# Kernel tuning notes

Hardware: AMD Instinct MI355X
Metric: run time of the kernel (lower is better)

## Reference

```python
import jax, jax.numpy as jnp
import numpy as np

N, E = 50000, 800000
DIN_N, DIN_E = 64, 64
DO_N, DO_E, H = 32, 32, 4
NEG_SLOPE = 0.01


def setup_inputs() -> dict:
    key = jax.random.key(0)
    ks = jax.random.split(key, 12)
    s = 0.05
    return {
        "nfeats": jax.random.normal(ks[0], (N, DIN_N), jnp.float32),
        "efeats": jax.random.normal(ks[1], (E, DIN_E), jnp.float32),
        "src": jax.random.randint(ks[2], (E,), 0, N, jnp.int32),
        "dst": jax.random.randint(ks[3], (E,), 0, N, jnp.int32),
        "Wn": jax.random.normal(ks[4], (DIN_N, DO_N * H), jnp.float32) * s,
        "bn": jnp.zeros((DO_N * H,), jnp.float32),
        "We": jax.random.normal(ks[5], (DIN_E + 2 * DIN_N, DO_E * H), jnp.float32) * s,
        "Wa": jax.random.normal(ks[6], (DO_E, H), jnp.float32) * s,
        "Won": jax.random.normal(ks[7], (DO_N * H, DO_N), jnp.float32) * s,
        "bon": jnp.zeros((DO_N,), jnp.float32),
        "Woe": jax.random.normal(ks[8], (DO_E * H, DO_E), jnp.float32) * s,
        "boe": jnp.zeros((DO_E,), jnp.float32),
    }


def _egat(nfeats, efeats, src, dst, Wn, bn, We, Wa, Won, bon, Woe, boe):
    # edge attention: concat [h_src, f, h_dst] -> linear(no bias) -> leaky_relu
    stack = jnp.concatenate([nfeats[src], efeats, nfeats[dst]], axis=-1)  # [E, 2Dn+De]
    f = jax.nn.leaky_relu(stack @ We, NEG_SLOPE).reshape(E, H, DO_E)      # [E, H, Fo]
    # fc_attn: [E,H,Fo] @ [Fo,H] -> [E,H,H], summed over last axis -> [E,H]
    a = jnp.einsum("ehf,fk->eh", f, Wa * 1.0) * 0 + (f @ Wa).sum(-1)
    a = (f @ Wa).sum(-1)  # [E, H]
    # projected node features for messages
    nproj = (nfeats @ Wn + bn).reshape(N, H, DO_N)  # [N, H, Do]
    # segment softmax of a over destination nodes
    m = jax.ops.segment_max(a, dst, num_segments=N)  # [N, H]
    m = jnp.where(jnp.isfinite(m), m, 0.0)
    ex = jnp.exp(a - m[dst])                         # [E, H]
    den = jax.ops.segment_sum(ex, dst, num_segments=N)  # [N, H]
    alpha = ex / den[dst]                            # safe: dst has >=1 edge here
    # weighted scatter-sum of src messages
    msg = alpha[:, :, None] * nproj[src]             # [E, H, Do]
    agg = jax.ops.segment_sum(msg, dst, num_segments=N)  # [N, H, Do]
    # zero in-degree nodes keep projected features (DGL update_all semantics)
    deg = jax.ops.segment_sum(jnp.ones((E,), nfeats.dtype), dst, num_segments=N)
    h = jnp.where(deg[:, None, None] > 0, agg, nproj)
    h_out = h.reshape(N, H * DO_N) @ Won + bon
    e_out = f.reshape(E, H * DO_E) @ Woe + boe
    return h_out, e_out


def reference(nfeats, efeats, src, dst, Wn, bn, We, Wa, Won, bon, Woe, boe):
    return _egat(nfeats, efeats, src, dst, Wn, bn, We, Wa, Won, bon, Woe, boe)
```

## Files before the change

kernel.cpp:

```cpp
#include <hip/hip_runtime.h>
#include <hip/hip_bf16.h>


#define NN 50000
#define NE 800000
#define NB ((NN + 255) / 256)

typedef __attribute__((ext_vector_type(8))) __bf16 bf16x8;
typedef __attribute__((ext_vector_type(4))) float f32x4;

__device__ __forceinline__ float lrelu(float x) { return x > 0.f ? x : 0.01f * x; }

__global__ __launch_bounds__(256) void k_count(const int* __restrict__ dst,
                                               int* __restrict__ deg)
{
    int i = blockIdx.x * blockDim.x + threadIdx.x;
    int stride = gridDim.x * blockDim.x;
    for (; i < NE; i += stride) atomicAdd(&deg[dst[i]], 1);
}

__global__ __launch_bounds__(256) void k_scan_blk(const int* __restrict__ deg,
                                                  int* __restrict__ rowptr,
                                                  int* __restrict__ bsum)
{
    __shared__ int wsum[4];
    const int tid = threadIdx.x, lane = tid & 63, wid = tid >> 6;
    const int i = blockIdx.x * 256 + tid;
    int v = (i < NN) ? deg[i] : 0;
    int x = v;
    #pragma unroll
    for (int off = 1; off < 64; off <<= 1) {
        int t = __shfl_up(x, off);
        if (lane >= off) x += t;
    }
    if (lane == 63) wsum[wid] = x;
    __syncthreads();
    if (tid == 0) {
        int s = 0;
        #pragma unroll
        for (int w = 0; w < 4; ++w) { int t = wsum[w]; wsum[w] = s; s += t; }
        bsum[blockIdx.x] = s;
    }
    __syncthreads();
    if (i < NN) rowptr[i] = wsum[wid] + x - v;
}

__global__ __launch_bounds__(256) void k_scan_top(int* __restrict__ bsum,
                                                  int* __restrict__ rowptr)
{
    __shared__ int wsum[4];
    const int tid = threadIdx.x, lane = tid & 63, wid = tid >> 6;
    int v = (tid < NB) ? bsum[tid] : 0;
    int x = v;
    #pragma unroll
    for (int off = 1; off < 64; off <<= 1) {
        int t = __shfl_up(x, off);
        if (lane >= off) x += t;
    }
    if (lane == 63) wsum[wid] = x;
    __syncthreads();
    if (tid == 0) {
        int s = 0;
        #pragma unroll
        for (int w = 0; w < 4; ++w) { int t = wsum[w]; wsum[w] = s; s += t; }
    }
    __syncthreads();
    int excl = wsum[wid] + x - v;
    if (tid < NB) bsum[tid] = excl;
    if (tid == NB - 1) rowptr[NN] = excl + v;
}

__global__ __launch_bounds__(256) void k_scan_add(int* __restrict__ rowptr,
                                                  const int* __restrict__ bsum,
                                                  int* __restrict__ cursor)
{
    const int i = blockIdx.x * 256 + threadIdx.x;
    if (i < NN) {
        int r = rowptr[i] + bsum[blockIdx.x];
        rowptr[i] = r;
        cursor[i] = r;
    }
}

__global__ __launch_bounds__(256) void k_prepw(const float* __restrict__ We,
                                               const float* __restrict__ Wa,
                                               unsigned short* __restrict__ Wefrag,
                                               float* __restrict__ wa_sum)
{
    const int tid = threadIdx.x;
    if (tid < 32) {
        float4 w = *reinterpret_cast<const float4*>(&Wa[tid * 4]);
        wa_sum[tid] = w.x + w.y + w.z + w.w;
    }
    #pragma unroll
    for (int i = 0; i < 32; ++i) {
        int idx = tid * 32 + i;
        int j = idx & 7, l = (idx >> 3) & 63, th = idx >> 9;
        int h = th & 1, t = th >> 1;
        int k = 32 * h + (l >> 4) * 8 + j;
        int c = 16 * t + (l & 15);
        __bf16 b = (__bf16)We[(64 + k) * 128 + c];
        Wefrag[idx] = *reinterpret_cast<unsigned short*>(&b);
    }
}

__global__ __launch_bounds__(256) void k_proj(
    const float* __restrict__ nf, const float* __restrict__ Wn,
    const float* __restrict__ bn, const float* __restrict__ We,
    float* __restrict__ nproj, float* __restrict__ Psrc, float* __restrict__ Pdst)
{
    __shared__ __align__(16) float sA[64 * 68];
    __shared__ __align__(16) float sW[64 * 128];
    const int tid = threadIdx.x;
    const int mode = blockIdx.y;
    const int nBase = blockIdx.x * 64;

    const float* W = (mode == 0) ? Wn : (mode == 1 ? We : We + 128 * 128);
    float* outp = (mode == 0) ? nproj : (mode == 1 ? Psrc : Pdst);

    #pragma unroll
    for (int q = 0; q < 4; ++q) {
        int idx = q * 256 + tid;
        int e = idx >> 4, c4 = idx & 15;
        int row = nBase + e;
        float4 v = make_float4(0.f, 0.f, 0.f, 0.f);
        if (row < NN) v = *reinterpret_cast<const float4*>(&nf[row * 64 + c4 * 4]);
        *reinterpret_cast<float4*>(&sA[e * 68 + c4 * 4]) = v;
    }
    #pragma unroll
    for (int q = 0; q < 8; ++q) {
        int idx = q * 256 + tid;
        *reinterpret_cast<float4*>(&sW[idx * 4]) =
            *reinterpret_cast<const float4*>(&W[idx * 4]);
    }
    __syncthreads();

    const int jt = tid & 15, et = tid >> 4;
    float acc[4][8];
    #pragma unroll
    for (int i = 0; i < 4; ++i)
        #pragma unroll
        for (int j = 0; j < 8; ++j) acc[i][j] = 0.f;

    #pragma unroll 2
    for (int kk4 = 0; kk4 < 16; ++kk4) {
        float4 a4[4];
        #pragma unroll
        for (int i = 0; i < 4; ++i)
            a4[i] = *reinterpret_cast<const float4*>(&sA[(4 * et + i) * 68 + 4 * kk4]);
        #pragma unroll
        for (int c = 0; c < 4; ++c) {
            int kk = 4 * kk4 + c;
            float4 b0 = *reinterpret_cast<const float4*>(&sW[kk * 128 + 4 * jt]);
            float4 b1 = *reinterpret_cast<const float4*>(&sW[kk * 128 + 64 + 4 * jt]);
            #pragma unroll
            for (int i = 0; i < 4; ++i) {
                float av = (&a4[i].x)[c];
                acc[i][0] = fmaf(av, b0.x, acc[i][0]);
                acc[i][1] = fmaf(av, b0.y, acc[i][1]);
                acc[i][2] = fmaf(av, b0.z, acc[i][2]);
                acc[i][3] = fmaf(av, b0.w, acc[i][3]);
                acc[i][4] = fmaf(av, b1.x, acc[i][4]);
                acc[i][5] = fmaf(av, b1.y, acc[i][5]);
                acc[i][6] = fmaf(av, b1.z, acc[i][6]);
                acc[i][7] = fmaf(av, b1.w, acc[i][7]);
            }
        }
    }

    float4 bias0 = make_float4(0.f, 0.f, 0.f, 0.f), bias1 = bias0;
    if (mode == 0) {
        bias0 = *reinterpret_cast<const float4*>(&bn[4 * jt]);
        bias1 = *reinterpret_cast<const float4*>(&bn[64 + 4 * jt]);
    }
    #pragma unroll
    for (int i = 0; i < 4; ++i) {
        int row = nBase + 4 * et + i;
        if (row >= NN) continue;
        float4 r0 = make_float4(acc[i][0] + bias0.x, acc[i][1] + bias0.y,
                                acc[i][2] + bias0.z, acc[i][3] + bias0.w);
        float4 r1 = make_float4(acc[i][4] + bias1.x, acc[i][5] + bias1.y,
                                acc[i][6] + bias1.z, acc[i][7] + bias1.w);
        *reinterpret_cast<float4*>(&outp[row * 128 + 4 * jt]) = r0;
        *reinterpret_cast<float4*>(&outp[row * 128 + 64 + 4 * jt]) = r1;
    }
}

__global__ __launch_bounds__(256) void k_edge(
    const float* __restrict__ ef, const int* __restrict__ src,
    const int* __restrict__ dst,
    const unsigned short* __restrict__ Wefrag, const float* __restrict__ wa_sum,
    const float* __restrict__ Woe, const float* __restrict__ boe,
    const float* __restrict__ Psrc, const float* __restrict__ Pdst,
    int* __restrict__ cursor, int* __restrict__ srcs,
    float* __restrict__ exs, float* __restrict__ e_out)
{
    __shared__ __align__(16) float sf[64 * 132];
    __shared__ __align__(16) float sWoe[128 * 32];
    __shared__ __align__(16) float sboe[32];

    const int tid = threadIdx.x;
    const int w = tid >> 6, l = tid & 63;
    const int g = l >> 4, c16 = l & 15;
    const int eBase = blockIdx.x * 64;
    const int rowBase = eBase + 16 * w;

    #pragma unroll
    for (int q = 0; q < 4; ++q) {
        int idx = q * 256 + tid;
        *reinterpret_cast<float4*>(&sWoe[idx * 4]) =
            *reinterpret_cast<const float4*>(&Woe[idx * 4]);
    }
    if (tid < 32) sboe[tid] = boe[tid];

    int sreg[4], dreg[4];
    #pragma unroll
    for (int r = 0; r < 4; ++r) {
        sreg[r] = src[rowBase + 4 * g + r];
        dreg[r] = dst[rowBase + 4 * g + r];
    }

    bf16x8 afrag[2];
    #pragma unroll
    for (int h = 0; h < 2; ++h) {
        const float* ap = &ef[(size_t)(rowBase + c16) * 64 + 32 * h + 8 * g];
        float4 a0 = *reinterpret_cast<const float4*>(ap);
        float4 a1 = *reinterpret_cast<const float4*>(ap + 4);
        bf16x8 v;
        v[0] = (__bf16)a0.x; v[1] = (__bf16)a0.y;
        v[2] = (__bf16)a0.z; v[3] = (__bf16)a0.w;
        v[4] = (__bf16)a1.x; v[5] = (__bf16)a1.y;
        v[6] = (__bf16)a1.z; v[7] = (__bf16)a1.w;
        afrag[h] = v;
    }

    f32x4 acc[8];
    #pragma unroll
    for (int t = 0; t < 8; ++t) {
        f32x4 z = {0.f, 0.f, 0.f, 0.f};
        acc[t] = z;
        #pragma unroll
        for (int h = 0; h < 2; ++h) {
            bf16x8 b = *reinterpret_cast<const bf16x8*>(
                &Wefrag[((size_t)(t * 2 + h) * 64 + l) * 8]);
            acc[t] = __builtin_amdgcn_mfma_f32_16x16x32_bf16(afrag[h], b, acc[t], 0, 0, 0);
        }
    }

    float a_acc[4][4];
    #pragma unroll
    for (int r = 0; r < 4; ++r)
        #pragma unroll
        for (int h = 0; h < 4; ++h) a_acc[r][h] = 0.f;

    #pragma unroll
    for (int t = 0; t < 8; ++t) {
        int j = 16 * t + c16;
        float waj = wa_sum[j & 31];
        #pragma unroll
        for (int r = 0; r < 4; ++r) {
            float ps = Psrc[(size_t)sreg[r] * 128 + j];
            float pd = Pdst[(size_t)dreg[r] * 128 + j];
            float f = lrelu(acc[t][r] + ps + pd);
            sf[(16 * w + 4 * g + r) * 132 + j] = f;
            a_acc[r][t >> 1] = fmaf(f, waj, a_acc[r][t >> 1]);
        }
    }

    #pragma unroll
    for (int r = 0; r < 4; ++r)
        #pragma unroll
        for (int h = 0; h < 4; ++h) {
            float v = a_acc[r][h];
            v += __shfl_xor(v, 1);
            v += __shfl_xor(v, 2);
            v += __shfl_xor(v, 4);
            v += __shfl_xor(v, 8);
            a_acc[r][h] = v;
        }

    #pragma unroll
    for (int r = 0; r < 4; ++r) {
        int pos = 0;
        if (c16 == 0) pos = atomicAdd(&cursor[dreg[r]], 1);
        pos = __shfl(pos, g * 16);
        if (c16 == 0) srcs[pos] = sreg[r];
        float ex = expf(a_acc[r][c16 & 3]);
        if (c16 < 4) exs[(size_t)pos * 4 + c16] = ex;
    }

    __syncthreads();

    {
        int e = tid >> 2, q = tid & 3;
        int j0 = q * 8;
        float4 r0 = make_float4(0.f, 0.f, 0.f, 0.f), r1 = r0;
        #pragma unroll 4
        for (int k = 0; k < 128; k += 4) {
            float4 fv = *reinterpret_cast<const float4*>(&sf[e * 132 + k]);
            #pragma unroll
            for (int c = 0; c < 4; ++c) {
                float fk = (&fv.x)[c];
                float4 w0 = *reinterpret_cast<const float4*>(&sWoe[(k + c) * 32 + j0]);
                float4 w1 = *reinterpret_cast<const float4*>(&sWoe[(k + c) * 32 + j0 + 4]);
                r0.x = fmaf(fk, w0.x, r0.x); r0.y = fmaf(fk, w0.y, r0.y);
                r0.z = fmaf(fk, w0.z, r0.z); r0.w = fmaf(fk, w0.w, r0.w);
                r1.x = fmaf(fk, w1.x, r1.x); r1.y = fmaf(fk, w1.y, r1.y);
                r1.z = fmaf(fk, w1.z, r1.z); r1.w = fmaf(fk, w1.w, r1.w);
            }
        }
        float4 b0 = *reinterpret_cast<const float4*>(&sboe[j0]);
        float4 b1 = *reinterpret_cast<const float4*>(&sboe[j0 + 4]);
        r0.x += b0.x; r0.y += b0.y; r0.z += b0.z; r0.w += b0.w;
        r1.x += b1.x; r1.y += b1.y; r1.z += b1.z; r1.w += b1.w;
        size_t o = (size_t)(eBase + e) * 32 + j0;
        *reinterpret_cast<float4*>(&e_out[o]) = r0;
        *reinterpret_cast<float4*>(&e_out[o + 4]) = r1;
    }
}

__global__ __launch_bounds__(256) void k_agg(
    const int* __restrict__ rowptr, const int* __restrict__ srcs,
    const float* __restrict__ exs, const float* __restrict__ nproj,
    float* __restrict__ hbuf)
{
    const int tid = threadIdx.x;
    const int j = tid & 127;
    const int n = blockIdx.x * 2 + (tid >> 7);
    if (n >= NN) return;
    const int beg = rowptr[n], end = rowptr[n + 1];
    const int h = j >> 5;
    float val = 0.f, den = 0.f;
    int s_next = (beg < end) ? srcs[beg] : 0;
    for (int p = beg; p < end; ++p) {
        int s = s_next;
        if (p + 1 < end) s_next = srcs[p + 1];
        float ex = exs[(size_t)p * 4 + h];
        val = fmaf(ex, nproj[(size_t)s * 128 + j], val);
        den += ex;
    }
    float out = (end > beg) ? (val / den) : nproj[(size_t)n * 128 + j];
    hbuf[(size_t)n * 128 + j] = out;
}

__global__ __launch_bounds__(256) void k_node_out(
    const float* __restrict__ hbuf, const float* __restrict__ Won,
    const float* __restrict__ bon, float* __restrict__ h_out)
{
    __shared__ __align__(16) float sh[64 * 132];
    __shared__ __align__(16) float sWon[128 * 32];
    __shared__ __align__(16) float sbon[32];
    const int tid = threadIdx.x;
    const int nBase = blockIdx.x * 64;

    #pragma unroll
    for (int q = 0; q < 8; ++q) {
        int idx = q * 256 + tid;
        int n = idx >> 5, c4 = idx & 31;
        int row = nBase + n;
        float4 v = make_float4(0.f, 0.f, 0.f, 0.f);
        if (row < NN)
            v = *reinterpret_cast<const float4*>(&hbuf[(size_t)row * 128 + c4 * 4]);
        *reinterpret_cast<float4*>(&sh[n * 132 + c4 * 4]) = v;
    }
    #pragma unroll
    for (int q = 0; q < 4; ++q) {
        int idx = q * 256 + tid;
        *reinterpret_cast<float4*>(&sWon[idx * 4]) =
            *reinterpret_cast<const float4*>(&Won[idx * 4]);
    }
    if (tid < 32) sbon[tid] = bon[tid];
    __syncthreads();

    int n = tid >> 2, q = tid & 3;
    int j0 = q * 8;
    int row = nBase + n;
    float4 r0 = make_float4(0.f, 0.f, 0.f, 0.f), r1 = r0;
    #pragma unroll 4
    for (int k = 0; k < 128; k += 4) {
        float4 fv = *reinterpret_cast<const float4*>(&sh[n * 132 + k]);
        #pragma unroll
        for (int c = 0; c < 4; ++c) {
            float fk = (&fv.x)[c];
            float4 w0 = *reinterpret_cast<const float4*>(&sWon[(k + c) * 32 + j0]);
            float4 w1 = *reinterpret_cast<const float4*>(&sWon[(k + c) * 32 + j0 + 4]);
            r0.x = fmaf(fk, w0.x, r0.x); r0.y = fmaf(fk, w0.y, r0.y);
            r0.z = fmaf(fk, w0.z, r0.z); r0.w = fmaf(fk, w0.w, r0.w);
            r1.x = fmaf(fk, w1.x, r1.x); r1.y = fmaf(fk, w1.y, r1.y);
            r1.z = fmaf(fk, w1.z, r1.z); r1.w = fmaf(fk, w1.w, r1.w);
        }
    }
    if (row < NN) {
        float4 b0 = *reinterpret_cast<const float4*>(&sbon[j0]);
        float4 b1 = *reinterpret_cast<const float4*>(&sbon[j0 + 4]);
        r0.x += b0.x; r0.y += b0.y; r0.z += b0.z; r0.w += b0.w;
        r1.x += b1.x; r1.y += b1.y; r1.z += b1.z; r1.w += b1.w;
        size_t o = (size_t)row * 32 + j0;
        *reinterpret_cast<float4*>(&h_out[o]) = r0;
        *reinterpret_cast<float4*>(&h_out[o + 4]) = r1;
    }
}

extern "C" void kernel_launch(void* const* d_in, const int* in_sizes, int n_in,
                              void* d_out, int out_size, void* d_ws, size_t ws_size,
                              hipStream_t stream) {
    const float* nfeats = (const float*)d_in[0];
    const float* efeats = (const float*)d_in[1];
    const int*   src    = (const int*)d_in[2];
    const int*   dst    = (const int*)d_in[3];
    const float* Wn     = (const float*)d_in[4];
    const float* bn     = (const float*)d_in[5];
    const float* We     = (const float*)d_in[6];
    const float* Wa     = (const float*)d_in[7];
    const float* Won    = (const float*)d_in[8];
    const float* bon    = (const float*)d_in[9];
    const float* Woe    = (const float*)d_in[10];
    const float* boe    = (const float*)d_in[11];

    float* h_out = (float*)d_out;
    float* e_out = h_out + (size_t)NN * 32;

    float* nproj  = (float*)d_ws;
    float* Psrc   = nproj + (size_t)NN * 128;
    float* Pdst   = Psrc + (size_t)NN * 128;
    float* exs    = Pdst + (size_t)NN * 128;
    int*   deg    = (int*)(exs + (size_t)NE * 4);
    int*   rowptr = deg + NN;
    int*   cursor = rowptr + NN + 1;
    int*   srcs   = cursor + NN;
    int*   bsum   = srcs + NE;
    float* wa_sum = (float*)(bsum + 256);
    unsigned short* Wefrag =
        (unsigned short*)(((uintptr_t)(wa_sum + 32) + 15) & ~(uintptr_t)15);
    float* hbuf   = Psrc;

    hipMemsetAsync(deg, 0, NN * sizeof(int), stream);

    k_count<<<1024, 256, 0, stream>>>(dst, deg);
    k_scan_blk<<<NB, 256, 0, stream>>>(deg, rowptr, bsum);
    k_scan_top<<<1, 256, 0, stream>>>(bsum, rowptr);
    k_scan_add<<<NB, 256, 0, stream>>>(rowptr, bsum, cursor);

    k_prepw<<<1, 256, 0, stream>>>(We, Wa, Wefrag, wa_sum);

    dim3 gProj((NN + 63) / 64, 3);
    k_proj<<<gProj, 256, 0, stream>>>(nfeats, Wn, bn, We, nproj, Psrc, Pdst);

    k_edge<<<NE / 64, 256, 0, stream>>>(efeats, src, dst, Wefrag, wa_sum,
                                        Woe, boe, Psrc, Pdst,
                                        cursor, srcs, exs, e_out);

    k_agg<<<(NN + 1) / 2, 256, 0, stream>>>(rowptr, srcs, exs, nproj, hbuf);

    k_node_out<<<(NN + 63) / 64, 256, 0, stream>>>(hbuf, Won, bon, h_out);
}
```

Before: 779.7 us.

## Use bf16 MFMA for edge output projection and vectorize Psrc/Pdst gathers

Moves the per-edge f @ Woe projection from scalar FP32 FMAs over shared memory onto bf16 MFMA instructions, with Woe pre-packed into fragment layout in the prep kernel. The intermediate edge features are staged in shared memory as bf16, which shrinks LDS use and may raise occupancy. The Psrc/Pdst gathers change from scalar per-lane loads to float4 loads per edge quarter, and one atomic per edge is issued from a restructured thread mapping. Rounding the MFMA accumulator to bf16 before adding the node projections, and feeding bf16 features into the output matmul, lowers precision.

```diff
diff --git a/kernel.cpp b/kernel.cpp
--- a/kernel.cpp
+++ b/kernel.cpp
@@ -10,6 +10,12 @@
 typedef __attribute__((ext_vector_type(4))) float f32x4;
 
 __device__ __forceinline__ float lrelu(float x) { return x > 0.f ? x : 0.01f * x; }
+__device__ __forceinline__ unsigned short f2bf(float x) {
+    __bf16 b = (__bf16)x; return *reinterpret_cast<unsigned short*>(&b);
+}
+__device__ __forceinline__ float bf2f(unsigned short u) {
+    __bf16 b = *reinterpret_cast<__bf16*>(&u); return (float)b;
+}
 
 __global__ __launch_bounds__(256) void k_count(const int* __restrict__ dst,
                                                int* __restrict__ deg)
@@ -84,7 +90,9 @@
 
 __global__ __launch_bounds__(256) void k_prepw(const float* __restrict__ We,
                                                const float* __restrict__ Wa,
+                                               const float* __restrict__ Woe,
                                                unsigned short* __restrict__ Wefrag,
+                                               unsigned short* __restrict__ Woefrag,
                                                float* __restrict__ wa_sum)
 {
     const int tid = threadIdx.x;
@@ -92,15 +100,19 @@
         float4 w = *reinterpret_cast<const float4*>(&Wa[tid * 4]);
         wa_sum[tid] = w.x + w.y + w.z + w.w;
     }
-    #pragma unroll
-    for (int i = 0; i < 32; ++i) {
-        int idx = tid * 32 + i;
+    for (int idx = tid; idx < 8192; idx += 256) {
         int j = idx & 7, l = (idx >> 3) & 63, th = idx >> 9;
         int h = th & 1, t = th >> 1;
         int k = 32 * h + (l >> 4) * 8 + j;
         int c = 16 * t + (l & 15);
-        __bf16 b = (__bf16)We[(64 + k) * 128 + c];
-        Wefrag[idx] = *reinterpret_cast<unsigned short*>(&b);
+        Wefrag[idx] = f2bf(We[(64 + k) * 128 + c]);
+    }
+    for (int idx = tid; idx < 4096; idx += 256) {
+        int j = idx & 7, l = (idx >> 3) & 63, uk = idx >> 9;
+        int ks = uk & 3, u = uk >> 2;
+        int k = 32 * ks + (l >> 4) * 8 + j;
+        int c = 16 * u + (l & 15);
+        Woefrag[idx] = f2bf(Woe[k * 32 + c]);
     }
 }
 
@@ -189,15 +201,17 @@
 __global__ __launch_bounds__(256) void k_edge(
     const float* __restrict__ ef, const int* __restrict__ src,
     const int* __restrict__ dst,
-    const unsigned short* __restrict__ Wefrag, const float* __restrict__ wa_sum,
-    const float* __restrict__ Woe, const float* __restrict__ boe,
+    const unsigned short* __restrict__ Wefrag,
+    const unsigned short* __restrict__ Woefrag,
+    const float* __restrict__ wa_sum,
+    const float* __restrict__ boe,
     const float* __restrict__ Psrc, const float* __restrict__ Pdst,
     int* __restrict__ cursor, int* __restrict__ srcs,
     float* __restrict__ exs, float* __restrict__ e_out)
 {
-    __shared__ __align__(16) float sf[64 * 132];
-    __shared__ __align__(16) float sWoe[128 * 32];
-    __shared__ __align__(16) float sboe[32];
+    __shared__ __align__(16) unsigned short fbuf[64 * 136];
+    __shared__ __align__(16) int sidx[128];
+    __shared__ __align__(16) float swa[32];
 
     const int tid = threadIdx.x;
     const int w = tid >> 6, l = tid & 63;
@@ -205,20 +219,8 @@
     const int eBase = blockIdx.x * 64;
     const int rowBase = eBase + 16 * w;
 
-    #pragma unroll
-    for (int q = 0; q < 4; ++q) {
-        int idx = q * 256 + tid;
-        *reinterpret_cast<float4*>(&sWoe[idx * 4]) =
-            *reinterpret_cast<const float4*>(&Woe[idx * 4]);
-    }
-    if (tid < 32) sboe[tid] = boe[tid];
-
-    int sreg[4], dreg[4];
-    #pragma unroll
-    for (int r = 0; r < 4; ++r) {
-        sreg[r] = src[rowBase + 4 * g + r];
-        dreg[r] = dst[rowBase + 4 * g + r];
-    }
+    if (tid < 64) { sidx[tid] = src[eBase + tid]; sidx[64 + tid] = dst[eBase + tid]; }
+    else if (tid < 96) swa[tid - 64] = wa_sum[tid - 64];
 
     bf16x8 afrag[2];
     #pragma unroll
@@ -247,75 +249,78 @@
         }
     }
 
-    float a_acc[4][4];
-    #pragma unroll
-    for (int r = 0; r < 4; ++r)
-        #pragma unroll
-        for (int h = 0; h < 4; ++h) a_acc[r][h] = 0.f;
-
-    #pragma unroll
-    for (int t = 0; t < 8; ++t) {
-        int j = 16 * t + c16;
-        float waj = wa_sum[j & 31];
-        #pragma unroll
-        for (int r = 0; r < 4; ++r) {
-            float ps = Psrc[(size_t)sreg[r] * 128 + j];
-            float pd = Pdst[(size_t)dreg[r] * 128 + j];
-            float f = lrelu(acc[t][r] + ps + pd);
-            sf[(16 * w + 4 * g + r) * 132 + j] = f;
-            a_acc[r][t >> 1] = fmaf(f, waj, a_acc[r][t >> 1]);
-        }
-    }
-
-    #pragma unroll
-    for (int r = 0; r < 4; ++r)
+    #pragma unroll
+    for (int t = 0; t < 8; ++t)
+        #pragma unroll
+        for (int r = 0; r < 4; ++r)
+            fbuf[(16 * w + 4 * g + r) * 136 + 16 * t + c16] = f2bf(acc[t][r]);
+
+    __syncthreads();
+
+    {
+        const int e = tid >> 2, q = tid & 3;
+        const int s = sidx[e], d = sidx[64 + e];
+        float4 wlo = *reinterpret_cast<const float4*>(&swa[4 * q]);
+        float4 whi = *reinterpret_cast<const float4*>(&swa[16 + 4 * q]);
+        float ah[4] = {0.f, 0.f, 0.f, 0.f};
+        #pragma unroll
+        for (int j = 0; j < 8; ++j) {
+            int col = 16 * j + 4 * q;
+            float4 ps = *reinterpret_cast<const float4*>(&Psrc[(size_t)s * 128 + col]);
+            float4 pd = *reinterpret_cast<const float4*>(&Pdst[(size_t)d * 128 + col]);
+            ushort4 rw = *reinterpret_cast<const ushort4*>(&fbuf[e * 136 + col]);
+            float f0 = lrelu(bf2f(rw.x) + ps.x + pd.x);
+            float f1 = lrelu(bf2f(rw.y) + ps.y + pd.y);
+            float f2 = lrelu(bf2f(rw.z) + ps.z + pd.z);
+            float f3 = lrelu(bf2f(rw.w) + ps.w + pd.w);
+            const float4& wv = (j & 1) ? whi : wlo;
+            int h = j >> 1;
+            ah[h] = fmaf(f0, wv.x, ah[h]);
+            ah[h] = fmaf(f1, wv.y, ah[h]);
+            ah[h] = fmaf(f2, wv.z, ah[h]);
+            ah[h] = fmaf(f3, wv.w, ah[h]);
+            ushort4 fw;
+            fw.x = f2bf(f0); fw.y = f2bf(f1); fw.z = f2bf(f2); fw.w = f2bf(f3);
+            *reinterpret_cast<ushort4*>(&fbuf[e * 136 + col]) = fw;
+        }
         #pragma unroll
         for (int h = 0; h < 4; ++h) {
-            float v = a_acc[r][h];
+            float v = ah[h];
             v += __shfl_xor(v, 1);
             v += __shfl_xor(v, 2);
-            v += __shfl_xor(v, 4);
-            v += __shfl_xor(v, 8);
-            a_acc[r][h] = v;
-        }
-
-    #pragma unroll
-    for (int r = 0; r < 4; ++r) {
+            ah[h] = v;
+        }
         int pos = 0;
-        if (c16 == 0) pos = atomicAdd(&cursor[dreg[r]], 1);
-        pos = __shfl(pos, g * 16);
-        if (c16 == 0) srcs[pos] = sreg[r];
-        float ex = expf(a_acc[r][c16 & 3]);
-        if (c16 < 4) exs[(size_t)pos * 4 + c16] = ex;
+        if (q == 0) pos = atomicAdd(&cursor[d], 1);
+        pos = __shfl(pos, l & ~3);
+        if (q == 0) srcs[pos] = s;
+        float myA = (q == 0) ? ah[0] : (q == 1) ? ah[1] : (q == 2) ? ah[2] : ah[3];
+        exs[(size_t)pos * 4 + q] = expf(myA);
     }
 
     __syncthreads();
 
     {
-        int e = tid >> 2, q = tid & 3;
-        int j0 = q * 8;
-        float4 r0 = make_float4(0.f, 0.f, 0.f, 0.f), r1 = r0;
-        #pragma unroll 4
-        for (int k = 0; k < 128; k += 4) {
-            float4 fv = *reinterpret_cast<const float4*>(&sf[e * 132 + k]);
+        bf16x8 af[4];
+        #pragma unroll
+        for (int ks = 0; ks < 4; ++ks)
+            af[ks] = *reinterpret_cast<const bf16x8*>(
+                &fbuf[(16 * w + c16) * 136 + 32 * ks + 8 * g]);
+        #pragma unroll
+        for (int u = 0; u < 2; ++u) {
+            f32x4 o = {0.f, 0.f, 0.f, 0.f};
             #pragma unroll
-            for (int c = 0; c < 4; ++c) {
-                float fk = (&fv.x)[c];
-                float4 w0 = *reinterpret_cast<const float4*>(&sWoe[(k + c) * 32 + j0]);
-                float4 w1 = *reinterpret_cast<const float4*>(&sWoe[(k + c) * 32 + j0 + 4]);
-                r0.x = fmaf(fk, w0.x, r0.x); r0.y = fmaf(fk, w0.y, r0.y);
-                r0.z = fmaf(fk, w0.z, r0.z); r0.w = fmaf(fk, w0.w, r0.w);
-                r1.x = fmaf(fk, w1.x, r1.x); r1.y = fmaf(fk, w1.y, r1.y);
-                r1.z = fmaf(fk, w1.z, r1.z); r1.w = fmaf(fk, w1.w, r1.w);
+            for (int ks = 0; ks < 4; ++ks) {
+                bf16x8 b = *reinterpret_cast<const bf16x8*>(
+                    &Woefrag[((size_t)(u * 4 + ks) * 64 + l) * 8]);
+                o = __builtin_amdgcn_mfma_f32_16x16x32_bf16(af[ks], b, o, 0, 0, 0);
             }
-        }
-        float4 b0 = *reinterpret_cast<const float4*>(&sboe[j0]);
-        float4 b1 = *reinterpret_cast<const float4*>(&sboe[j0 + 4]);
-        r0.x += b0.x; r0.y += b0.y; r0.z += b0.z; r0.w += b0.w;
-        r1.x += b1.x; r1.y += b1.y; r1.z += b1.z; r1.w += b1.w;
-        size_t o = (size_t)(eBase + e) * 32 + j0;
-        *reinterpret_cast<float4*>(&e_out[o]) = r0;
-        *reinterpret_cast<float4*>(&e_out[o + 4]) = r1;
+            float bo = boe[16 * u + c16];
+            #pragma unroll
+            for (int r = 0; r < 4; ++r)
+                e_out[(size_t)(eBase + 16 * w + 4 * g + r) * 32 + 16 * u + c16] =
+                    o[r] + bo;
+        }
     }
 }
 
@@ -432,6 +437,7 @@
     float* wa_sum = (float*)(bsum + 256);
     unsigned short* Wefrag =
         (unsigned short*)(((uintptr_t)(wa_sum + 32) + 15) & ~(uintptr_t)15);
+    unsigned short* Woefrag = Wefrag + 8192;
     float* hbuf   = Psrc;
 
     hipMemsetAsync(deg, 0, NN * sizeof(int), stream);
@@ -441,13 +447,13 @@
     k_scan_top<<<1, 256, 0, stream>>>(bsum, rowptr);
     k_scan_add<<<NB, 256, 0, stream>>>(rowptr, bsum, cursor);
 
-    k_prepw<<<1, 256, 0, stream>>>(We, Wa, Wefrag, wa_sum);
+    k_prepw<<<1, 256, 0, stream>>>(We, Wa, Woe, Wefrag, Woefrag, wa_sum);
 
     dim3 gProj((NN + 63) / 64, 3);
     k_proj<<<gProj, 256, 0, stream>>>(nfeats, Wn, bn, We, nproj, Psrc, Pdst);
 
-    k_edge<<<NE / 64, 256, 0, stream>>>(efeats, src, dst, Wefrag, wa_sum,
-                                        Woe, boe, Psrc, Pdst,
+    k_edge<<<NE / 64, 256, 0, stream>>>(efeats, src, dst, Wefrag, Woefrag,
+                                        wa_sum, boe, Psrc, Pdst,
                                         cursor, srcs, exs, e_out);
 
     k_agg<<<(NN + 1) / 2, 256, 0, stream>>>(rowptr, srcs, exs, nproj, hbuf);
```

Measured after the change: 708.4 us. 1.1x faster.
